# Optimization experiments

Measured on AMD Instinct MI355X. Metric: run time of the kernel, lower is better.

The kernel has to match this reference:

```python
import jax, jax.numpy as jnp
import numpy as np

K = 3          # kernel size
PAD = 1        # padding
# deformable conv v2: offset conv (2*K*K ch), modulator conv (K*K ch, 2*sigmoid), main 3x3 conv, ReLU


def _conv2d(x, w, b):
    y = jax.lax.conv_general_dilated(x, w, (1, 1), ((PAD, PAD), (PAD, PAD)),
                                     dimension_numbers=('NCHW', 'OIHW', 'NCHW'))
    return y + b[None, :, None, None]


def _bilinear_gather(x, py, px):
    # x: [B,C,H,W]; py/px: [B,K2,H,W] float sample coords; zero outside image.
    B, C, H, W = x.shape
    y0 = jnp.floor(py)
    x0 = jnp.floor(px)
    wy1 = py - y0
    wx1 = px - x0
    wy0 = 1.0 - wy1
    wx0 = 1.0 - wx1
    xf = x.reshape(B, C, H * W)

    def gather(yi, xi):
        valid = (yi >= 0) & (yi <= H - 1) & (xi >= 0) & (xi <= W - 1)
        yc = jnp.clip(yi, 0, H - 1).astype(jnp.int32)
        xc = jnp.clip(xi, 0, W - 1).astype(jnp.int32)
        idx = (yc * W + xc).reshape(B, -1)                      # [B, K2*H*W]
        v = jax.vmap(lambda xb, ib: xb[:, ib])(xf, idx)         # [B, C, K2*H*W]
        v = v.reshape(B, C, *yi.shape[1:])                      # [B, C, K2, H, W]
        return v * valid[:, None].astype(x.dtype)

    return (gather(y0, x0) * (wy0 * wx0)[:, None]
            + gather(y0, x0 + 1) * (wy0 * wx1)[:, None]
            + gather(y0 + 1, x0) * (wy1 * wx0)[:, None]
            + gather(y0 + 1, x0 + 1) * (wy1 * wx1)[:, None])


def _deform_conv(data, w, b, w_off, b_off, w_mod, b_mod):
    B, Cin, H, W = data.shape
    off = _conv2d(data, w_off, b_off)                           # [B, 2*K2, H, W]
    mask = 2.0 * jax.nn.sigmoid(_conv2d(data, w_mod, b_mod))    # [B, K2, H, W]
    off = off.reshape(B, K * K, 2, H, W)                        # (dy, dx) per tap
    dy, dx = off[:, :, 0], off[:, :, 1]
    ki, kj = jnp.meshgrid(jnp.arange(K), jnp.arange(K), indexing='ij')
    ki = ki.reshape(-1).astype(data.dtype)
    kj = kj.reshape(-1).astype(data.dtype)
    hs = jnp.arange(H, dtype=data.dtype)
    ws = jnp.arange(W, dtype=data.dtype)
    py = hs[None, None, :, None] - PAD + ki[None, :, None, None] + dy
    px = ws[None, None, None, :] - PAD + kj[None, :, None, None] + dx
    sampled = _bilinear_gather(data, py, px)                    # [B, Cin, K2, H, W]
    sampled = sampled * mask[:, None]
    out = jnp.einsum('bckhw,ock->bohw', sampled, w.reshape(w.shape[0], Cin, K * K))
    return out + b[None, :, None, None]


def setup_inputs() -> dict:
    key = jax.random.key(0)
    ks = jax.random.split(key, 7)
    B, Cin, Cout, H, W = 8, 64, 64, 128, 128
    fan = Cin * K * K
    return {
        'data': jax.random.normal(ks[0], (B, Cin, H, W), jnp.float32),
        'w': jax.random.normal(ks[1], (Cout, Cin, K, K), jnp.float32) / np.sqrt(fan),
        'b': jax.random.normal(ks[2], (Cout,), jnp.float32) * 0.01,
        'w_off': jax.random.normal(ks[3], (2 * K * K, Cin, K, K), jnp.float32) * (0.1 / np.sqrt(fan)),
        'b_off': jnp.zeros((2 * K * K,), jnp.float32),
        'w_mod': jax.random.normal(ks[4], (K * K, Cin, K, K), jnp.float32) * (0.1 / np.sqrt(fan)),
        'b_mod': jnp.zeros((K * K,), jnp.float32),
    }


def reference(data, w, b, w_off, b_off, w_mod, b_mod):
    return jax.nn.relu(_deform_conv(data, w, b, w_off, b_off, w_mod, b_mod))
```

## Files before the change

### kernel.cpp

```cpp
#include <hip/hip_runtime.h>
#include <hip/hip_fp16.h>
#include <cstdint>


typedef _Float16 half8 __attribute__((ext_vector_type(8)));
typedef __attribute__((ext_vector_type(4))) float floatx4;

__device__ __forceinline__ unsigned int pack2h(float lo, float hi) {
    __half2 h = __floats2half2_rn(lo, hi);
    union { __half2 h; unsigned int u; } cv; cv.h = h;
    return cv.u;
}
__device__ __forceinline__ unsigned int blend2h(unsigned int a, unsigned int b,
                                                unsigned int c, unsigned int d,
                                                const __half2* w) {
    union { unsigned int u; __half2 h; } A, B, C, D, O;
    A.u = a; B.u = b; C.u = c; D.u = d;
    __half2 s = __hmul2(A.h, w[0]);
    s = __hfma2(B.h, w[1], s);
    s = __hfma2(C.h, w[2], s);
    s = __hfma2(D.h, w[3], s);
    O.h = s;
    return O.u;
}

#define OFF_DATAT 0u
#define OFF_OFFP  16777216u
#define OFF_WM    30932992u
#define OFF_W27   31006720u
#define OFF_B27   31043584u

__global__ __launch_bounds__(256) void prep_k(const float* __restrict__ x,
                                              unsigned short* __restrict__ xt,
                                              const float* __restrict__ w,
                                              const float* __restrict__ w_off,
                                              const float* __restrict__ w_mod,
                                              const float* __restrict__ b_off,
                                              const float* __restrict__ b_mod,
                                              unsigned short* __restrict__ wpackM,
                                              unsigned short* __restrict__ wpack27,
                                              float* __restrict__ bias27) {
    __shared__ float tile[64][65];
    int blk = blockIdx.x;
    if (blk < 2048) {
        int b    = blk >> 8;
        int pos0 = (blk & 255) << 6;
        int lane = threadIdx.x & 63;
        int g    = threadIdx.x >> 6;
        for (int c = g; c < 64; c += 4)
            tile[c][lane] = x[(((b << 6) + c) << 14) + pos0 + lane];
        __syncthreads();
        int c2 = lane & 31;
        for (int i = g; i < 32; i += 4) {
            int pr = (i << 1) + (lane >> 5);
            unsigned int d = pack2h(tile[c2 << 1][pr], tile[(c2 << 1) + 1][pr]);
            *(unsigned int*)&xt[((size_t)((b << 14) + pos0 + pr) << 6) + (c2 << 1)] = d;
        }
        return;
    }
    int t = (blk - 2048) * 256 + threadIdx.x;
    if (t < 64 * 576) {
        int o = t / 576, kk = t % 576;
        int k = kk >> 6, c = kk & 63;
        __half hv = __float2half_rn(w[(o * 64 + c) * 9 + k]);
        wpackM[t] = __half_as_ushort(hv);
        return;
    }
    t -= 64 * 576;
    if (t < 32 * 576) {
        int o = t / 576, kk = t % 576;
        int k = kk >> 6, c = kk & 63;
        float v = 0.f;
        if (o < 18)      v = w_off[(o * 64 + c) * 9 + k];
        else if (o < 27) v = w_mod[((o - 18) * 64 + c) * 9 + k];
        wpack27[t] = __half_as_ushort(__float2half_rn(v));
        if (kk == 0) bias27[o] = (o < 18) ? b_off[o] : (o < 27 ? b_mod[o - 18] : 0.f);
    }
}

__global__ __launch_bounds__(256) void conv27_k(const unsigned short* __restrict__ xt,
                                                const unsigned short* __restrict__ wpack27,
                                                const float* __restrict__ bias27,
                                                float* __restrict__ offP) {
    __shared__ unsigned short tile[4][66][72];
    int blk   = blockIdx.x;
    int b     = blk >> 7;
    int patch = blk & 127;
    int m     = patch >> 1;
    int h     = patch & 1;
    int tid   = threadIdx.x;
    int lane  = tid & 63, wv = tid >> 6;
    int r = lane & 15, q = lane >> 4;

    const unsigned short* xb = xt + ((size_t)b << 20);

    {
        int g = tid >> 3, j = tid & 7;
        #pragma unroll
        for (int rr = 0; rr < 4; ++rr) {
            int sy = (m << 1) + rr - 1;
            #pragma unroll
            for (int ci = 0; ci < 3; ++ci) {
                int col = g + (ci << 5);
                if (col < 66) {
                    int sx = (h << 6) + col - 1;
                    uint4 v = {0u, 0u, 0u, 0u};
                    if (sy >= 0 && sy < 128 && sx >= 0 && sx < 128)
                        v = *(const uint4*)&xb[(size_t)(((sy << 7) + sx) << 6) + (j << 3)];
                    *(uint4*)&tile[rr][col][j << 3] = v;
                }
            }
        }
    }
    __syncthreads();

    floatx4 acc[4] = {};
    #pragma unroll
    for (int k = 0; k < 9; ++k) {
        int ki = k / 3, kj = k % 3;
        #pragma unroll
        for (int ch = 0; ch < 2; ++ch) {
            half8 a0 = *(const half8*)&wpack27[(r)      * 576 + (k << 6) + (ch << 5) + (q << 3)];
            half8 a1 = *(const half8*)&wpack27[(16 + r) * 576 + (k << 6) + (ch << 5) + (q << 3)];
            #pragma unroll
            for (int tr = 0; tr < 2; ++tr) {
                half8 bfrag = *(const half8*)&tile[tr + ki][(wv << 4) + r + kj][(ch << 5) + (q << 3)];
                acc[0 + tr] = __builtin_amdgcn_mfma_f32_16x16x32_f16(a0, bfrag, acc[0 + tr], 0, 0, 0);
                acc[2 + tr] = __builtin_amdgcn_mfma_f32_16x16x32_f16(a1, bfrag, acc[2 + tr], 0, 0, 0);
            }
        }
    }

    #pragma unroll
    for (int s = 0; s < 2; ++s) {
        #pragma unroll
        for (int tr = 0; tr < 2; ++tr) {
            #pragma unroll
            for (int reg = 0; reg < 4; ++reg) {
                int oc = (s << 4) + (q << 2) + reg;
                if (oc >= 27) continue;
                int pos = (((m << 1) + tr) << 7) + (h << 6) + (wv << 4) + r;
                float v = acc[(s << 1) + tr][reg] + bias27[oc];
                int kk, comp;
                if (oc < 18) { kk = oc >> 1; comp = oc & 1; }
                else         { kk = oc - 18; comp = 2; v = 2.f / (1.f + __expf(-v)); }
                offP[(size_t)(((b * 9 + kk) * 3 + comp) << 14) + pos] = v;
            }
        }
    }
}

__global__ __launch_bounds__(256, 5) void deform_main_k(const unsigned short* __restrict__ xt,
                                                        const unsigned short* __restrict__ wpackM,
                                                        const float* __restrict__ offP,
                                                        const float* __restrict__ bias,
                                                        float* __restrict__ out) {
    __shared__ ushort4 pOff[576];
    __shared__ uint4   pW[576];
    __shared__ unsigned short samp[2][64][72];
    int blk  = blockIdx.x;
    int b    = blk >> 8;
    int pos0 = (blk & 255) << 6;
    int tid  = threadIdx.x;
    int lane = tid & 63, wv = tid >> 6;
    int r = lane & 15, q = lane >> 4;
    int pg = lane >> 3;
    int j8 = lane & 7;

    const char* xbb = (const char*)(xt + ((size_t)b << 20));

    for (int e = tid; e < 576; e += 256) {
        int k = e >> 6, p = e & 63;
        int pos = pos0 + p;
        const float* offk = offP + ((size_t)((b * 9 + k) * 3) << 14);
        float dy = offk[pos];
        float dx = offk[16384 + pos];
        float m  = offk[32768 + pos];
        float py = (float)(pos >> 7) + (float)(k / 3 - 1) + dy;
        float px = (float)(pos & 127) + (float)(k % 3 - 1) + dx;
        float y0f = floorf(py), x0f = floorf(px);
        int y0 = (int)y0f, x0 = (int)x0f;
        float wy1 = py - y0f, wx1 = px - x0f;
        float wy0 = 1.f - wy1, wx0 = 1.f - wx1;
        bool vy0 = (y0 >= 0) && (y0 < 128);
        bool vy1 = (y0 >= -1) && (y0 < 127);
        bool vx0 = (x0 >= 0) && (x0 < 128);
        bool vx1 = (x0 >= -1) && (x0 < 127);
        float w00 = (vy0 && vx0) ? m * wy0 * wx0 : 0.f;
        float w01 = (vy0 && vx1) ? m * wy0 * wx1 : 0.f;
        float w10 = (vy1 && vx0) ? m * wy1 * wx0 : 0.f;
        float w11 = (vy1 && vx1) ? m * wy1 * wx1 : 0.f;
        int y0c = min(max(y0, 0), 127), y1c = min(max(y0 + 1, 0), 127);
        int x0c = min(max(x0, 0), 127), x1c = min(max(x0 + 1, 0), 127);
        ushort4 io;
        io.x = (unsigned short)((y0c << 7) + x0c);
        io.y = (unsigned short)((y0c << 7) + x1c);
        io.z = (unsigned short)((y1c << 7) + x0c);
        io.w = (unsigned short)((y1c << 7) + x1c);
        pOff[e] = io;
        union { uint4 u; __half2 h[4]; } pw;
        pw.h[0] = __float2half2_rn(w00);
        pw.h[1] = __float2half2_rn(w01);
        pw.h[2] = __float2half2_rn(w10);
        pw.h[3] = __float2half2_rn(w11);
        pW[e] = pw.u;
    }
    __syncthreads();

    floatx4 acc[4] = {};
    const char* xp = xbb + (j8 << 4);
    const unsigned short* wrow = wpackM + ((wv << 4) + r) * 576 + (q << 3);

    uint4   c00[2], c01[2], c10[2], c11[2];
    ushort4 pio[2];
    uint4   pcw[2];
    uint4   cw[2];
    half8   afC[2], afN[2];

    auto readParams = [&](int k) {
        #pragma unroll
        for (int i = 0; i < 2; ++i) {
            int e  = (k << 6) + (wv << 4) + (i << 3) + pg;
            pio[i] = pOff[e];
            pcw[i] = pW[e];
        }
    };
    auto issue = [&]() {
        #pragma unroll
        for (int i = 0; i < 2; ++i) {
            cw[i]  = pcw[i];
            c00[i] = *(const uint4*)(xp + ((int)pio[i].x << 7));
            c01[i] = *(const uint4*)(xp + ((int)pio[i].y << 7));
            c10[i] = *(const uint4*)(xp + ((int)pio[i].z << 7));
            c11[i] = *(const uint4*)(xp + ((int)pio[i].w << 7));
        }
    };
    auto blendStore = [&](int buf) {
        #pragma unroll
        for (int i = 0; i < 2; ++i) {
            int p = (wv << 4) + (i << 3) + pg;
            union { uint4 u; __half2 h[4]; } W; W.u = cw[i];
            uint4 o4;
            o4.x = blend2h(c00[i].x, c01[i].x, c10[i].x, c11[i].x, W.h);
            o4.y = blend2h(c00[i].y, c01[i].y, c10[i].y, c11[i].y, W.h);
            o4.z = blend2h(c00[i].z, c01[i].z, c10[i].z, c11[i].z, W.h);
            o4.w = blend2h(c00[i].w, c01[i].w, c10[i].w, c11[i].w, W.h);
            *(uint4*)&samp[buf][p][j8 << 3] = o4;
        }
    };

    readParams(0);
    issue();
    afC[0] = *(const half8*)&wrow[0];
    afC[1] = *(const half8*)&wrow[32];
    blendStore(0);
    readParams(1);

    for (int k = 0; k < 9; ++k) {
        if (k < 8) {
            issue();
            afN[0] = *(const half8*)&wrow[((k + 1) << 6)];
            afN[1] = *(const half8*)&wrow[((k + 1) << 6) + 32];
        }
        __syncthreads();
        #pragma unroll
        for (int ch = 0; ch < 2; ++ch) {
            #pragma unroll
            for (int nt = 0; nt < 4; ++nt) {
                half8 bfrag = *(const half8*)&samp[k & 1][(nt << 4) + r][(ch << 5) + (q << 3)];
                acc[nt] = __builtin_amdgcn_mfma_f32_16x16x32_f16(afC[ch], bfrag, acc[nt], 0, 0, 0);
            }
        }
        if (k < 8) {
            blendStore((k + 1) & 1);
            if (k < 7) readParams(k + 2);
            afC[0] = afN[0];
            afC[1] = afN[1];
        }
    }

    #pragma unroll
    for (int nt = 0; nt < 4; ++nt) {
        #pragma unroll
        for (int reg = 0; reg < 4; ++reg) {
            int oc  = (wv << 4) + (q << 2) + reg;
            int pos = pos0 + (nt << 4) + r;
            float v = acc[nt][reg] + bias[oc];
            out[(size_t)(((b << 6) + oc) << 14) + pos] = fmaxf(v, 0.f);
        }
    }
}

extern "C" void kernel_launch(void* const* d_in, const int* in_sizes, int n_in,
                              void* d_out, int out_size, void* d_ws, size_t ws_size,
                              hipStream_t stream) {
    const float* data  = (const float*)d_in[0];
    const float* w     = (const float*)d_in[1];
    const float* bias  = (const float*)d_in[2];
    const float* w_off = (const float*)d_in[3];
    const float* b_off = (const float*)d_in[4];
    const float* w_mod = (const float*)d_in[5];
    const float* b_mod = (const float*)d_in[6];
    float* out = (float*)d_out;

    char* ws = (char*)d_ws;
    unsigned short* dataT   = (unsigned short*)(ws + OFF_DATAT);
    float*          offP    = (float*)(ws + OFF_OFFP);
    unsigned short* wpackM  = (unsigned short*)(ws + OFF_WM);
    unsigned short* wpack27 = (unsigned short*)(ws + OFF_W27);
    float*          bias27  = (float*)(ws + OFF_B27);

    prep_k<<<2264, 256, 0, stream>>>(data, dataT, w, w_off, w_mod,
                                     b_off, b_mod, wpackM, wpack27, bias27);
    conv27_k<<<1024, 256, 0, stream>>>(dataT, wpack27, bias27, offP);
    deform_main_k<<<2048, 256, 0, stream>>>(dataT, wpackM, offP, bias, out);
}
```

Before: 159.9 us.

## Deepen bilinear gather prefetch to two taps ahead in deform conv main kernel

The main deformable-conv kernel now keeps two taps of bilinear corner loads in flight, using double-buffered register slots, instead of one. The tap loop is fully unrolled so the slot indices are resolved at compile time. Launch bounds drop from 5 to 3 blocks per SM to make room for the extra registers. The aim is to hide more gather latency per wave, at the cost of fewer resident waves to hide latency across blocks.

```diff
diff --git a/kernel.cpp b/kernel.cpp
--- a/kernel.cpp
+++ b/kernel.cpp
@@ -62,8 +62,7 @@
     if (t < 64 * 576) {
         int o = t / 576, kk = t % 576;
         int k = kk >> 6, c = kk & 63;
-        __half hv = __float2half_rn(w[(o * 64 + c) * 9 + k]);
-        wpackM[t] = __half_as_ushort(hv);
+        wpackM[t] = __half_as_ushort(__float2half_rn(w[(o * 64 + c) * 9 + k]));
         return;
     }
     t -= 64 * 576;
@@ -150,7 +149,7 @@
     }
 }
 
-__global__ __launch_bounds__(256, 5) void deform_main_k(const unsigned short* __restrict__ xt,
+__global__ __launch_bounds__(256, 3) void deform_main_k(const unsigned short* __restrict__ xt,
                                                         const unsigned short* __restrict__ wpackM,
                                                         const float* __restrict__ offP,
                                                         const float* __restrict__ bias,
@@ -211,54 +210,55 @@
     const char* xp = xbb + (j8 << 4);
     const unsigned short* wrow = wpackM + ((wv << 4) + r) * 576 + (q << 3);
 
-    uint4   c00[2], c01[2], c10[2], c11[2];
-    ushort4 pio[2];
-    uint4   pcw[2];
-    uint4   cw[2];
+    uint4   c00[2][2], c01[2][2], c10[2][2], c11[2][2];
+    uint4   cwS[2][2];
+    ushort4 nio[2];
+    uint4   ncw[2];
     half8   afC[2], afN[2];
 
     auto readParams = [&](int k) {
         #pragma unroll
         for (int i = 0; i < 2; ++i) {
             int e  = (k << 6) + (wv << 4) + (i << 3) + pg;
-            pio[i] = pOff[e];
-            pcw[i] = pW[e];
+            nio[i] = pOff[e];
+            ncw[i] = pW[e];
         }
     };
-    auto issue = [&]() {
+    auto issueInto = [&](int s) {
         #pragma unroll
         for (int i = 0; i < 2; ++i) {
-            cw[i]  = pcw[i];
-            c00[i] = *(const uint4*)(xp + ((int)pio[i].x << 7));
-            c01[i] = *(const uint4*)(xp + ((int)pio[i].y << 7));
-            c10[i] = *(const uint4*)(xp + ((int)pio[i].z << 7));
-            c11[i] = *(const uint4*)(xp + ((int)pio[i].w << 7));
+            cwS[s][i] = ncw[i];
+            c00[s][i] = *(const uint4*)(xp + ((int)nio[i].x << 7));
+            c01[s][i] = *(const uint4*)(xp + ((int)nio[i].y << 7));
+            c10[s][i] = *(const uint4*)(xp + ((int)nio[i].z << 7));
+            c11[s][i] = *(const uint4*)(xp + ((int)nio[i].w << 7));
         }
     };
-    auto blendStore = [&](int buf) {
+    auto blendStore = [&](int s, int buf) {
         #pragma unroll
         for (int i = 0; i < 2; ++i) {
             int p = (wv << 4) + (i << 3) + pg;
-            union { uint4 u; __half2 h[4]; } W; W.u = cw[i];
+            union { uint4 u; __half2 h[4]; } W; W.u = cwS[s][i];
             uint4 o4;
-            o4.x = blend2h(c00[i].x, c01[i].x, c10[i].x, c11[i].x, W.h);
-            o4.y = blend2h(c00[i].y, c01[i].y, c10[i].y, c11[i].y, W.h);
-            o4.z = blend2h(c00[i].z, c01[i].z, c10[i].z, c11[i].z, W.h);
-            o4.w = blend2h(c00[i].w, c01[i].w, c10[i].w, c11[i].w, W.h);
+            o4.x = blend2h(c00[s][i].x, c01[s][i].x, c10[s][i].x, c11[s][i].x, W.h);
+            o4.y = blend2h(c00[s][i].y, c01[s][i].y, c10[s][i].y, c11[s][i].y, W.h);
+            o4.z = blend2h(c00[s][i].z, c01[s][i].z, c10[s][i].z, c11[s][i].z, W.h);
+            o4.w = blend2h(c00[s][i].w, c01[s][i].w, c10[s][i].w, c11[s][i].w, W.h);
             *(uint4*)&samp[buf][p][j8 << 3] = o4;
         }
     };
 
-    readParams(0);
-    issue();
+    readParams(0); issueInto(0);
+    readParams(1); issueInto(1);
     afC[0] = *(const half8*)&wrow[0];
     afC[1] = *(const half8*)&wrow[32];
-    blendStore(0);
-    readParams(1);
-
+    blendStore(0, 0);
+    readParams(2);
+
+    #pragma unroll
     for (int k = 0; k < 9; ++k) {
+        if (k <= 6) issueInto(k & 1);
         if (k < 8) {
-            issue();
             afN[0] = *(const half8*)&wrow[((k + 1) << 6)];
             afN[1] = *(const half8*)&wrow[((k + 1) << 6) + 32];
         }
@@ -272,8 +272,8 @@
             }
         }
         if (k < 8) {
-            blendStore((k + 1) & 1);
-            if (k < 7) readParams(k + 2);
+            blendStore((k + 1) & 1, (k + 1) & 1);
+            if (k <= 5) readParams(k + 3);
             afC[0] = afN[0];
             afC[1] = afN[1];
         }
```

Measured after the change: 158.0 us. About the same (-1.2%).
